# Kernel optimization log

Measured on AMD Instinct MI355X. Metric: run time of the kernel, lower is better.

The kernel has to match this reference:

```python
import jax, jax.numpy as jnp
import numpy as np

B, S, H, NH, I, V, P, T = 8, 512, 768, 12, 3072, 30522, 512, 2
D = H // NH
EPS = 1e-12


def _ln(x, g, b):
    m = x.mean(-1, keepdims=True)
    v = ((x - m) ** 2).mean(-1, keepdims=True)
    return (x - m) / jnp.sqrt(v + EPS) * g + b


def setup_inputs() -> dict:
    key = jax.random.key(0)
    ks = jax.random.split(key, 24)
    s = 0.02
    f32 = jnp.float32
    d = {
        'x': jax.random.randint(ks[0], (B, S), 0, V, dtype=jnp.int32),
        'W_word': (jax.random.normal(ks[1], (V, H)) * s).astype(f32),
        'W_pos': (jax.random.normal(ks[2], (P, H)) * s).astype(f32),
        'W_type': (jax.random.normal(ks[3], (T, H)) * s).astype(f32),
        'g_emb': jnp.ones((H,), f32), 'b_emb': jnp.zeros((H,), f32),
        'Wq': (jax.random.normal(ks[4], (H, H)) * s).astype(f32), 'bq': jnp.zeros((H,), f32),
        'Wk': (jax.random.normal(ks[5], (H, H)) * s).astype(f32), 'bk': jnp.zeros((H,), f32),
        'Wv': (jax.random.normal(ks[6], (H, H)) * s).astype(f32), 'bv': jnp.zeros((H,), f32),
        'Wo': (jax.random.normal(ks[7], (H, H)) * s).astype(f32), 'bo': jnp.zeros((H,), f32),
        'g_attn': jnp.ones((H,), f32), 'b_attn': jnp.zeros((H,), f32),
        'Wi': (jax.random.normal(ks[8], (H, I)) * s).astype(f32), 'bi': jnp.zeros((I,), f32),
        'Wd': (jax.random.normal(ks[9], (I, H)) * s).astype(f32), 'bd': jnp.zeros((H,), f32),
        'g_out': jnp.ones((H,), f32), 'b_out': jnp.zeros((H,), f32),
        'Wp': (jax.random.normal(ks[10], (H, H)) * s).astype(f32), 'bp': jnp.zeros((H,), f32),
    }
    return d


def _forward(x, W_word, W_pos, W_type, g_emb, b_emb, Wq, bq, Wk, bk, Wv, bv,
             Wo, bo, g_attn, b_attn, Wi, bi, Wd, bd, g_out, b_out, Wp, bp):
    # embeddings: word + position(arange) + token_type(all zeros -> row 0)
    h = W_word[x] + W_pos[jnp.arange(S)][None, :, :] + W_type[0][None, None, :]
    h = _ln(h, g_emb, b_emb)
    scale = 1.0 / jnp.sqrt(jnp.float32(D))
    # NOTE: the torch module shares one set of layer weights across all 6 layers.
    for _ in range(6):
        q = (h @ Wq + bq).reshape(B, S, NH, D).transpose(0, 2, 1, 3)  # bhsd
        k = (h @ Wk + bk).reshape(B, S, NH, D).transpose(0, 2, 1, 3)
        v = (h @ Wv + bv).reshape(B, S, NH, D).transpose(0, 2, 1, 3)
        scores = jnp.einsum('bhqd,bhkd->bhqk', q, k) * scale
        probs = jax.nn.softmax(scores, axis=-1)
        ctx = jnp.einsum('bhqk,bhkd->bhqd', probs, v)
        ctx = ctx.transpose(0, 2, 1, 3).reshape(B, S, H)
        attn = ctx @ Wo + bo
        xa = _ln(h + attn, g_attn, b_attn)
        ff = jax.nn.gelu(xa @ Wi + bi, approximate=False) @ Wd + bd
        h = _ln(xa + ff, g_out, b_out)
    pooled = h[:, 0, :] @ Wp + bp  # no tanh in the original module
    return h, pooled


def reference(x, W_word, W_pos, W_type, g_emb, b_emb, Wq, bq, Wk, bk, Wv, bv,
              Wo, bo, g_attn, b_attn, Wi, bi, Wd, bd, g_out, b_out, Wp, bp):
    return _forward(x, W_word, W_pos, W_type, g_emb, b_emb, Wq, bq, Wk, bk, Wv, bv,
                    Wo, bo, g_attn, b_attn, Wi, bi, Wd, bd, g_out, b_out, Wp, bp)
```

## Files before the change

kernel.cpp:

```cpp
#include <hip/hip_runtime.h>
#include <hip/hip_bf16.h>
#include <math.h>

#define B_  8
#define S_  512
#define H_  768
#define NH_ 12
#define D_  64
#define I_  3072
#define NTOK (B_*S_)
#define LDQ 2304

typedef __attribute__((ext_vector_type(8))) __bf16 bf16x8;
typedef __attribute__((ext_vector_type(8))) unsigned short ushort8;
typedef __attribute__((ext_vector_type(4))) float  f32x4;

__device__ __forceinline__ float gelu_exact(float x) {
    return 0.5f * x * (1.0f + erff(x * 0.70710678118654752440f));
}

__device__ __forceinline__ unsigned short f2bf(float x) {
    __hip_bfloat16 h = __float2bfloat16(x);
    return *reinterpret_cast<unsigned short*>(&h);
}

__device__ __forceinline__ void gload16(const void* g, void* l) {
    __builtin_amdgcn_global_load_lds(
        (const __attribute__((address_space(1))) void*)g,
        (__attribute__((address_space(3))) void*)l,
        16, 0, 0);
}

__global__ void cvtT_kernel(const float* __restrict__ W, __hip_bfloat16* __restrict__ WT,
                            int K, int N) {
    __shared__ float tile[32][33];
    int k0 = blockIdx.y * 32, n0 = blockIdx.x * 32;
    int tx = threadIdx.x & 31, ty = threadIdx.x >> 5;
    #pragma unroll
    for (int i = 0; i < 32; i += 8)
        tile[ty + i][tx] = W[(long)(k0 + ty + i) * N + n0 + tx];
    __syncthreads();
    #pragma unroll
    for (int i = 0; i < 32; i += 8)
        WT[(long)(n0 + ty + i) * K + k0 + tx] = __float2bfloat16(tile[tx][ty + i]);
}

__global__ void embed_ln_kernel(const int* __restrict__ ids,
                                const float* __restrict__ Wword,
                                const float* __restrict__ Wpos,
                                const float* __restrict__ Wtype,
                                const float* __restrict__ g,
                                const float* __restrict__ b,
                                float* __restrict__ out,
                                __hip_bfloat16* __restrict__ outb) {
    int t = blockIdx.x;
    int s = t % S_;
    long id = ids[t];
    int tid = threadIdx.x;
    float vals[3];
    float sum = 0.f, sq = 0.f;
    #pragma unroll
    for (int i = 0; i < 3; ++i) {
        int c = tid + 256 * i;
        float e = Wword[id * H_ + c] + Wpos[(long)s * H_ + c] + Wtype[c];
        vals[i] = e; sum += e; sq += e * e;
    }
    __shared__ float r1[256], r2[256];
    r1[tid] = sum; r2[tid] = sq; __syncthreads();
    for (int st = 128; st > 0; st >>= 1) {
        if (tid < st) { r1[tid] += r1[tid + st]; r2[tid] += r2[tid + st]; }
        __syncthreads();
    }
    float mean = r1[0] * (1.0f / H_);
    float var  = r2[0] * (1.0f / H_) - mean * mean;
    float inv  = rsqrtf(var + 1e-12f);
    #pragma unroll
    for (int i = 0; i < 3; ++i) {
        int c = tid + 256 * i;
        float v = (vals[i] - mean) * inv * g[c] + b[c];
        out[(long)t * H_ + c] = v;
        outb[(long)t * H_ + c] = __float2bfloat16(v);
    }
}

__global__ void add_ln_kernel(const float* __restrict__ a,
                              const float* __restrict__ r,
                              const float* __restrict__ g,
                              const float* __restrict__ bb,
                              float* __restrict__ out,
                              __hip_bfloat16* __restrict__ outb) {
    int t = blockIdx.x;
    int tid = threadIdx.x;
    float vals[3];
    float sum = 0.f, sq = 0.f;
    #pragma unroll
    for (int i = 0; i < 3; ++i) {
        int c = tid + 256 * i;
        float e = a[(long)t * H_ + c] + r[(long)t * H_ + c];
        vals[i] = e; sum += e; sq += e * e;
    }
    __shared__ float r1[256], r2[256];
    r1[tid] = sum; r2[tid] = sq; __syncthreads();
    for (int st = 128; st > 0; st >>= 1) {
        if (tid < st) { r1[tid] += r1[tid + st]; r2[tid] += r2[tid + st]; }
        __syncthreads();
    }
    float mean = r1[0] * (1.0f / H_);
    float var  = r2[0] * (1.0f / H_) - mean * mean;
    float inv  = rsqrtf(var + 1e-12f);
    #pragma unroll
    for (int i = 0; i < 3; ++i) {
        int c = tid + 256 * i;
        float v = (vals[i] - mean) * inv * g[c] + bb[c];
        out[(long)t * H_ + c] = v;
        outb[(long)t * H_ + c] = __float2bfloat16(v);
    }
}

template<int BM, int BN, int MI, int NJ, int ACT, int WF32, int WB16>
__global__ __launch_bounds__(256, 3) void mfma_gemm_kernel(
    const __hip_bfloat16* __restrict__ A,
    const __hip_bfloat16* __restrict__ BT,
    const float* __restrict__ bias,
    float* __restrict__ Cf,
    __hip_bfloat16* __restrict__ Cb,
    int M, int N, int K) {
    constexpr int WC = BN / (NJ * 16);
    constexpr int WR = BM / (MI * 16);
    static_assert(WR * WC == 4, "4 waves");
    constexpr int LA = BM * 4 / 256;
    constexpr int LB = BN * 4 / 256;
    constexpr int L  = LA + LB;
    __shared__ __align__(16) __hip_bfloat16 sA[2][BM * 32];
    __shared__ __align__(16) __hip_bfloat16 sB[2][BN * 32];
    const int tid  = threadIdx.x;
    const int lane = tid & 63;
    const int w    = tid >> 6;
    const int wr   = w / WC, wc = w % WC;
    const int l15  = lane & 15, l4 = lane >> 4;
    const int m0 = blockIdx.y * BM, n0 = blockIdx.x * BN;

    auto stage = [&](int buf, int k0) {
        #pragma unroll
        for (int t = 0; t < LA; ++t) {
            int c = tid + 256 * t;
            gload16(A + (long)(m0 + (c >> 2)) * K + k0 + (c & 3) * 8, &sA[buf][c * 8]);
        }
        #pragma unroll
        for (int t = 0; t < LB; ++t) {
            int c = tid + 256 * t;
            gload16(BT + (long)(n0 + (c >> 2)) * K + k0 + (c & 3) * 8, &sB[buf][c * 8]);
        }
    };

    f32x4 acc[MI][NJ] = {};
    const int nk = K >> 5;

    stage(0, 0);
    for (int t = 0; t < nk; ++t) {
        const int cur = t & 1;
        if (t + 1 < nk) {
            stage(cur ^ 1, (t + 1) * 32);
            asm volatile("s_waitcnt vmcnt(%0)" :: "i"(L) : "memory");
        } else {
            asm volatile("s_waitcnt vmcnt(0)" ::: "memory");
        }
        __builtin_amdgcn_sched_barrier(0);
        __builtin_amdgcn_s_barrier();
        __builtin_amdgcn_sched_barrier(0);

        const int kk = l4 * 8;
        bf16x8 af[MI], bf[NJ];
        #pragma unroll
        for (int i = 0; i < MI; ++i)
            af[i] = *reinterpret_cast<const bf16x8*>(&sA[cur][(wr * MI * 16 + i * 16 + l15) * 32 + kk]);
        #pragma unroll
        for (int j = 0; j < NJ; ++j)
            bf[j] = *reinterpret_cast<const bf16x8*>(&sB[cur][(wc * NJ * 16 + j * 16 + l15) * 32 + kk]);
        #pragma unroll
        for (int i = 0; i < MI; ++i)
            #pragma unroll
            for (int j = 0; j < NJ; ++j)
                acc[i][j] = __builtin_amdgcn_mfma_f32_16x16x32_bf16(af[i], bf[j], acc[i][j], 0, 0, 0);

        __builtin_amdgcn_sched_barrier(0);
        __builtin_amdgcn_s_barrier();
        __builtin_amdgcn_sched_barrier(0);
    }

    #pragma unroll
    for (int i = 0; i < MI; ++i) {
        #pragma unroll
        for (int j = 0; j < NJ; ++j) {
            int col = n0 + wc * NJ * 16 + j * 16 + l15;
            float bv = bias[col];
            #pragma unroll
            for (int r = 0; r < 4; ++r) {
                int row = m0 + wr * MI * 16 + i * 16 + l4 * 4 + r;
                float v = acc[i][j][r] + bv;
                if (ACT == 1) v = gelu_exact(v);
                if (WF32) Cf[(long)row * N + col] = v;
                if (WB16) Cb[(long)row * N + col] = __float2bfloat16(v);
            }
        }
    }
}

__global__ __launch_bounds__(256, 4) void flash_attn_kernel(
    const __hip_bfloat16* __restrict__ QKV,
    __hip_bfloat16* __restrict__ Ctx) {
    __shared__ __align__(16) unsigned short sK[64 * 72];
    __shared__ __align__(16) unsigned short sVt[64 * 72];
    __shared__ __align__(16) unsigned short sP[4 * 16 * 72];

    const int tid  = threadIdx.x;
    const int lane = tid & 63;
    const int w    = tid >> 6;
    const int l15  = lane & 15, l4 = lane >> 4;
    const int qb = blockIdx.x;
    const int bh = blockIdx.y;
    const int b  = bh / NH_, hd = bh % NH_;
    const long rbase = (long)b * S_ * LDQ;
    const int qoff = hd * D_, koff = H_ + hd * D_, voff = 2 * H_ + hd * D_;

    const int qrow0 = qb * 64 + w * 16;
    bf16x8 af[2];
    #pragma unroll
    for (int ks = 0; ks < 2; ++ks)
        af[ks] = *reinterpret_cast<const bf16x8*>(
            QKV + rbase + (long)(qrow0 + l15) * LDQ + qoff + ks * 32 + l4 * 8);

    f32x4 ctx[4] = {};
    float m_run[4], l_run[4];
    #pragma unroll
    for (int r = 0; r < 4; ++r) { m_run[r] = -1e30f; l_run[r] = 0.f; }

    const int sr = tid >> 2;
    const int sc = (tid & 3) * 16;
    unsigned short* pl = sP + w * (16 * 72);

    for (int kv0 = 0; kv0 < S_; kv0 += 64) {
        const __hip_bfloat16* kg = QKV + rbase + (long)(kv0 + sr) * LDQ + koff + sc;
        const __hip_bfloat16* vg = QKV + rbase + (long)(kv0 + sr) * LDQ + voff + sc;
        ushort8 kv_a = *reinterpret_cast<const ushort8*>(kg);
        ushort8 kv_b = *reinterpret_cast<const ushort8*>(kg + 8);
        ushort8 vv_a = *reinterpret_cast<const ushort8*>(vg);
        ushort8 vv_b = *reinterpret_cast<const ushort8*>(vg + 8);
        __syncthreads();
        *reinterpret_cast<ushort8*>(sK + sr * 72 + sc)     = kv_a;
        *reinterpret_cast<ushort8*>(sK + sr * 72 + sc + 8) = kv_b;
        #pragma unroll
        for (int i = 0; i < 8; ++i) {
            sVt[(sc + i) * 72 + sr]     = vv_a[i];
            sVt[(sc + 8 + i) * 72 + sr] = vv_b[i];
        }
        __syncthreads();

        f32x4 s[4];
        #pragma unroll
        for (int j = 0; j < 4; ++j) {
            s[j] = (f32x4){0.f, 0.f, 0.f, 0.f};
            #pragma unroll
            for (int ks = 0; ks < 2; ++ks) {
                bf16x8 bk = *reinterpret_cast<const bf16x8*>(sK + (j * 16 + l15) * 72 + ks * 32 + l4 * 8);
                s[j] = __builtin_amdgcn_mfma_f32_16x16x32_bf16(af[ks], bk, s[j], 0, 0, 0);
            }
        }
        #pragma unroll
        for (int j = 0; j < 4; ++j) s[j] *= 0.125f;

        #pragma unroll
        for (int r = 0; r < 4; ++r) {
            float mx = fmaxf(fmaxf(s[0][r], s[1][r]), fmaxf(s[2][r], s[3][r]));
            #pragma unroll
            for (int o = 1; o < 16; o <<= 1) mx = fmaxf(mx, __shfl_xor(mx, o));
            float mnew = fmaxf(m_run[r], mx);
            float sum = 0.f;
            #pragma unroll
            for (int j = 0; j < 4; ++j) {
                float p = __expf(s[j][r] - mnew);
                s[j][r] = p; sum += p;
            }
            #pragma unroll
            for (int o = 1; o < 16; o <<= 1) sum += __shfl_xor(sum, o);
            float resc = __expf(m_run[r] - mnew);
            l_run[r] = l_run[r] * resc + sum;
            m_run[r] = mnew;
            #pragma unroll
            for (int j = 0; j < 4; ++j) ctx[j][r] *= resc;
        }

        #pragma unroll
        for (int j = 0; j < 4; ++j)
            #pragma unroll
            for (int r = 0; r < 4; ++r)
                pl[(l4 * 4 + r) * 72 + j * 16 + l15] = f2bf(s[j][r]);

        #pragma unroll
        for (int ks = 0; ks < 2; ++ks) {
            bf16x8 ap = *reinterpret_cast<const bf16x8*>(pl + l15 * 72 + ks * 32 + l4 * 8);
            #pragma unroll
            for (int jd = 0; jd < 4; ++jd) {
                bf16x8 bv = *reinterpret_cast<const bf16x8*>(sVt + (jd * 16 + l15) * 72 + ks * 32 + l4 * 8);
                ctx[jd] = __builtin_amdgcn_mfma_f32_16x16x32_bf16(ap, bv, ctx[jd], 0, 0, 0);
            }
        }
    }

    #pragma unroll
    for (int r = 0; r < 4; ++r) {
        float inv = 1.f / l_run[r];
        long tok = (long)b * S_ + qb * 64 + w * 16 + l4 * 4 + r;
        #pragma unroll
        for (int jd = 0; jd < 4; ++jd)
            Ctx[tok * H_ + hd * D_ + jd * 16 + l15] = __float2bfloat16(ctx[jd][r] * inv);
    }
}

__global__ void pooled_kernel(const float* __restrict__ h,
                              const float* __restrict__ Wp,
                              const float* __restrict__ bp,
                              float* __restrict__ out) {
    int b = blockIdx.y;
    int col = blockIdx.x * 256 + threadIdx.x;
    const float* hb = h + (long)b * S_ * H_;
    float acc = 0.f;
    #pragma unroll 8
    for (int k = 0; k < H_; ++k)
        acc += hb[k] * Wp[(long)k * H_ + col];
    out[(long)b * H_ + col] = acc + bp[col];
}

extern "C" void kernel_launch(void* const* d_in, const int* in_sizes, int n_in,
                              void* d_out, int out_size, void* d_ws, size_t ws_size,
                              hipStream_t stream) {
    const int*   x      = (const int*)  d_in[0];
    const float* W_word = (const float*)d_in[1];
    const float* W_pos  = (const float*)d_in[2];
    const float* W_type = (const float*)d_in[3];
    const float* g_emb  = (const float*)d_in[4];
    const float* b_emb  = (const float*)d_in[5];
    const float* Wq     = (const float*)d_in[6];
    const float* bq     = (const float*)d_in[7];
    const float* Wk     = (const float*)d_in[8];
    const float* bk     = (const float*)d_in[9];
    const float* Wv     = (const float*)d_in[10];
    const float* bv     = (const float*)d_in[11];
    const float* Wo     = (const float*)d_in[12];
    const float* bo     = (const float*)d_in[13];
    const float* g_attn = (const float*)d_in[14];
    const float* b_attn = (const float*)d_in[15];
    const float* Wi     = (const float*)d_in[16];
    const float* bi     = (const float*)d_in[17];
    const float* Wd     = (const float*)d_in[18];
    const float* bd     = (const float*)d_in[19];
    const float* g_out  = (const float*)d_in[20];
    const float* b_out  = (const float*)d_in[21];
    const float* Wp     = (const float*)d_in[22];
    const float* bp     = (const float*)d_in[23];

    const size_t NT = (size_t)NTOK * H_;
    char* base = (char*)d_ws;
    size_t off = 0;
    auto alloc = [&](size_t bytes) -> char* {
        char* p = base + off;
        off += (bytes + 255) & ~(size_t)255;
        return p;
    };
    float* h    = (float*)alloc(NT * 4);
    float* xa   = (float*)alloc(NT * 4);
    float* kb   = (float*)alloc(NT * 4);
    __hip_bfloat16* h_b   = (__hip_bfloat16*)alloc(NT * 2);
    __hip_bfloat16* xa_b  = (__hip_bfloat16*)alloc(NT * 2);
    __hip_bfloat16* qkv_b = (__hip_bfloat16*)alloc((size_t)NTOK * LDQ * 2);
    __hip_bfloat16* ctx_b = (__hip_bfloat16*)alloc(NT * 2);
    __hip_bfloat16* ff1_b = (__hip_bfloat16*)alloc((size_t)NTOK * I_ * 2);
    __hip_bfloat16* WqkvT = (__hip_bfloat16*)alloc((size_t)LDQ * H_ * 2);
    __hip_bfloat16* WoT = (__hip_bfloat16*)alloc((size_t)H_ * H_ * 2);
    __hip_bfloat16* WiT = (__hip_bfloat16*)alloc((size_t)H_ * I_ * 2);
    __hip_bfloat16* WdT = (__hip_bfloat16*)alloc((size_t)I_ * H_ * 2);
    float* bqkv = (float*)alloc(LDQ * 4);

    cvtT_kernel<<<dim3(H_/32, H_/32), 256, 0, stream>>>(Wq, WqkvT, H_, H_);
    cvtT_kernel<<<dim3(H_/32, H_/32), 256, 0, stream>>>(Wk, WqkvT + (size_t)H_ * H_, H_, H_);
    cvtT_kernel<<<dim3(H_/32, H_/32), 256, 0, stream>>>(Wv, WqkvT + (size_t)2 * H_ * H_, H_, H_);
    cvtT_kernel<<<dim3(H_/32, H_/32), 256, 0, stream>>>(Wo, WoT, H_, H_);
    cvtT_kernel<<<dim3(I_/32, H_/32), 256, 0, stream>>>(Wi, WiT, H_, I_);
    cvtT_kernel<<<dim3(H_/32, I_/32), 256, 0, stream>>>(Wd, WdT, I_, H_);
    hipMemcpyAsync(bqkv,          bq, H_ * 4, hipMemcpyDeviceToDevice, stream);
    hipMemcpyAsync(bqkv + H_,     bk, H_ * 4, hipMemcpyDeviceToDevice, stream);
    hipMemcpyAsync(bqkv + 2 * H_, bv, H_ * 4, hipMemcpyDeviceToDevice, stream);

    embed_ln_kernel<<<NTOK, 256, 0, stream>>>(x, W_word, W_pos, W_type, g_emb, b_emb, h, h_b);

    dim3 gqkv(LDQ/128, NTOK/128);
    dim3 g768(H_/64,  NTOK/128);
    dim3 gi(I_/128,  NTOK/128);
    for (int layer = 0; layer < 6; ++layer) {
        mfma_gemm_kernel<128,128,4,4,0,0,1><<<gqkv, 256, 0, stream>>>(
            h_b, WqkvT, bqkv, nullptr, qkv_b, NTOK, LDQ, H_);
        flash_attn_kernel<<<dim3(S_/64, B_*NH_), 256, 0, stream>>>(qkv_b, ctx_b);
        mfma_gemm_kernel<128,64,4,2,0,1,0><<<g768, 256, 0, stream>>>(
            ctx_b, WoT, bo, kb, nullptr, NTOK, H_, H_);
        add_ln_kernel<<<NTOK, 256, 0, stream>>>(h, kb, g_attn, b_attn, xa, xa_b);
        mfma_gemm_kernel<128,128,4,4,1,0,1><<<gi, 256, 0, stream>>>(
            xa_b, WiT, bi, nullptr, ff1_b, NTOK, I_, H_);
        mfma_gemm_kernel<128,64,4,2,0,1,0><<<g768, 256, 0, stream>>>(
            ff1_b, WdT, bd, kb, nullptr, NTOK, H_, I_);
        add_ln_kernel<<<NTOK, 256, 0, stream>>>(xa, kb, g_out, b_out, h, h_b);
    }

    hipMemcpyAsync(d_out, h, NT * sizeof(float), hipMemcpyDeviceToDevice, stream);
    pooled_kernel<<<dim3(3, 8), 256, 0, stream>>>(h, Wp, bp, (float*)d_out + NT);
}
```

Before: 1.182 ms.

## Add 256x256 tiled MFMA GEMM with swizzled LDS for QKV and FFN1

Adds a 512-thread GEMM kernel that computes a 256x256 output tile per block. It double-buffers two 32-wide K sub-stages in 128KB of dynamic LDS, uses XOR-swizzled LDS addressing to reduce bank conflicts, and raises wave priority around the MFMA bursts. The QKV and FFN1 projections use it when the large LDS allocation is accepted; otherwise they fall back to the 128x128 kernel. The goal is more operand reuse per byte loaded. The cost is far fewer blocks (144 and 192), which may leave many of the 256 CUs idle at one block per CU.

Result: slower. 1.208 ms (+2.2%).

```diff
diff --git a/kernel.cpp b/kernel.cpp
--- a/kernel.cpp
+++ b/kernel.cpp
@@ -30,6 +30,8 @@
         (__attribute__((address_space(3))) void*)l,
         16, 0, 0);
 }
+
+#define SB0() __builtin_amdgcn_sched_barrier(0)
 
 __global__ void cvtT_kernel(const float* __restrict__ W, __hip_bfloat16* __restrict__ WT,
                             int K, int N) {
@@ -114,6 +116,109 @@
         float v = (vals[i] - mean) * inv * g[c] + bb[c];
         out[(long)t * H_ + c] = v;
         outb[(long)t * H_ + c] = __float2bfloat16(v);
+    }
+}
+
+template<int ACT, int WF32, int WB16>
+__global__ __launch_bounds__(512, 1) void mfma_gemm256_kernel(
+    const __hip_bfloat16* __restrict__ A,
+    const __hip_bfloat16* __restrict__ BT,
+    const float* __restrict__ bias,
+    float* __restrict__ Cf,
+    __hip_bfloat16* __restrict__ Cb,
+    int M, int N, int K) {
+    extern __shared__ __align__(16) unsigned short smem[];
+    const int tid  = threadIdx.x;
+    const int lane = tid & 63;
+    const int w    = tid >> 6;
+    const int wr   = w >> 2;
+    const int wc   = w & 3;
+    const int l15  = lane & 15, l4 = lane >> 4;
+    const int m0 = blockIdx.y * 256, n0 = blockIdx.x * 256;
+    const int goff = (l15 >> 1) & 3;
+
+    auto stageA = [&](int buf, int s, int k0) {
+        #pragma unroll
+        for (int u = 0; u < 2; ++u) {
+            int c = tid + 512 * u;
+            int row = c >> 2, gq = c & 3;
+            int gsrc = gq ^ ((row >> 1) & 3);
+            gload16(A + (long)(m0 + row) * K + k0 + s * 32 + gsrc * 8,
+                    smem + (buf * 2 + s) * 8192 + row * 32 + gq * 8);
+        }
+    };
+    auto stageB = [&](int buf, int s, int k0) {
+        #pragma unroll
+        for (int u = 0; u < 2; ++u) {
+            int c = tid + 512 * u;
+            int row = c >> 2, gq = c & 3;
+            int gsrc = gq ^ ((row >> 1) & 3);
+            gload16(BT + (long)(n0 + row) * K + k0 + s * 32 + gsrc * 8,
+                    smem + 32768 + (buf * 2 + s) * 8192 + row * 32 + gq * 8);
+        }
+    };
+
+    f32x4 acc[8][4] = {};
+
+    auto comp = [&](int buf, int s) {
+        const unsigned short* pa = smem + (buf * 2 + s) * 8192;
+        const unsigned short* pb = smem + 32768 + (buf * 2 + s) * 8192;
+        const int gsw = (l4 ^ goff) * 8;
+        bf16x8 afr[8], bfr[4];
+        #pragma unroll
+        for (int mi = 0; mi < 8; ++mi)
+            afr[mi] = *reinterpret_cast<const bf16x8*>(pa + (wr * 128 + mi * 16 + l15) * 32 + gsw);
+        #pragma unroll
+        for (int nj = 0; nj < 4; ++nj)
+            bfr[nj] = *reinterpret_cast<const bf16x8*>(pb + (wc * 64 + nj * 16 + l15) * 32 + gsw);
+        __builtin_amdgcn_s_setprio(1);
+        #pragma unroll
+        for (int mi = 0; mi < 8; ++mi)
+            #pragma unroll
+            for (int nj = 0; nj < 4; ++nj)
+                acc[mi][nj] = __builtin_amdgcn_mfma_f32_16x16x32_bf16(afr[mi], bfr[nj], acc[mi][nj], 0, 0, 0);
+        __builtin_amdgcn_s_setprio(0);
+    };
+
+    const int nt = K >> 6;
+    stageA(0, 0, 0); stageB(0, 0, 0);
+    stageA(0, 1, 0); stageB(0, 1, 0);
+    SB0(); asm volatile("s_waitcnt vmcnt(4)" ::: "memory");
+    SB0(); __builtin_amdgcn_s_barrier(); SB0();
+
+    for (int t = 0; t < nt; ++t) {
+        const int cur = t & 1;
+        const int kn = (t + 1) << 6;
+        const bool more = (t + 1 < nt);
+        if (more) { stageA(cur ^ 1, 0, kn); stageB(cur ^ 1, 0, kn); }
+        comp(cur, 0);
+        SB0();
+        if (more) asm volatile("s_waitcnt vmcnt(4)" ::: "memory");
+        else      asm volatile("s_waitcnt vmcnt(0)" ::: "memory");
+        SB0(); __builtin_amdgcn_s_barrier(); SB0();
+        if (more) { stageA(cur ^ 1, 1, kn); stageB(cur ^ 1, 1, kn); }
+        comp(cur, 1);
+        if (more) {
+            SB0(); asm volatile("s_waitcnt vmcnt(4)" ::: "memory");
+            SB0(); __builtin_amdgcn_s_barrier(); SB0();
+        }
+    }
+
+    #pragma unroll
+    for (int mi = 0; mi < 8; ++mi) {
+        #pragma unroll
+        for (int nj = 0; nj < 4; ++nj) {
+            int col = n0 + wc * 64 + nj * 16 + l15;
+            float bv = bias[col];
+            #pragma unroll
+            for (int r = 0; r < 4; ++r) {
+                int row = m0 + wr * 128 + mi * 16 + l4 * 4 + r;
+                float v = acc[mi][nj][r] + bv;
+                if (ACT == 1) v = gelu_exact(v);
+                if (WF32) Cf[(long)row * N + col] = v;
+                if (WB16) Cb[(long)row * N + col] = __float2bfloat16(v);
+            }
+        }
     }
 }
 
@@ -165,9 +270,7 @@
         } else {
             asm volatile("s_waitcnt vmcnt(0)" ::: "memory");
         }
-        __builtin_amdgcn_sched_barrier(0);
-        __builtin_amdgcn_s_barrier();
-        __builtin_amdgcn_sched_barrier(0);
+        SB0(); __builtin_amdgcn_s_barrier(); SB0();
 
         const int kk = l4 * 8;
         bf16x8 af[MI], bf[NJ];
@@ -183,9 +286,7 @@
             for (int j = 0; j < NJ; ++j)
                 acc[i][j] = __builtin_amdgcn_mfma_f32_16x16x32_bf16(af[i], bf[j], acc[i][j], 0, 0, 0);
 
-        __builtin_amdgcn_sched_barrier(0);
-        __builtin_amdgcn_s_barrier();
-        __builtin_amdgcn_sched_barrier(0);
+        SB0(); __builtin_amdgcn_s_barrier(); SB0();
     }
 
     #pragma unroll
@@ -393,18 +494,35 @@
 
     embed_ln_kernel<<<NTOK, 256, 0, stream>>>(x, W_word, W_pos, W_type, g_emb, b_emb, h, h_b);
 
-    dim3 gqkv(LDQ/128, NTOK/128);
-    dim3 g768(H_/64,  NTOK/128);
-    dim3 gi(I_/128,  NTOK/128);
+    const int SMEM = 131072;
+    hipError_t e1 = hipFuncSetAttribute((const void*)mfma_gemm256_kernel<0,0,1>,
+                                        hipFuncAttributeMaxDynamicSharedMemorySize, SMEM);
+    hipError_t e2 = hipFuncSetAttribute((const void*)mfma_gemm256_kernel<1,0,1>,
+                                        hipFuncAttributeMaxDynamicSharedMemorySize, SMEM);
+    const bool big = (e1 == hipSuccess) && (e2 == hipSuccess);
+
+    dim3 gqkv128(LDQ/128, NTOK/128);
+    dim3 gi128(I_/128, NTOK/128);
+    dim3 gqkv256(LDQ/256, NTOK/256);
+    dim3 gi256(I_/256, NTOK/256);
+    dim3 g768(H_/64, NTOK/128);
     for (int layer = 0; layer < 6; ++layer) {
-        mfma_gemm_kernel<128,128,4,4,0,0,1><<<gqkv, 256, 0, stream>>>(
-            h_b, WqkvT, bqkv, nullptr, qkv_b, NTOK, LDQ, H_);
+        if (big)
+            mfma_gemm256_kernel<0,0,1><<<gqkv256, 512, SMEM, stream>>>(
+                h_b, WqkvT, bqkv, nullptr, qkv_b, NTOK, LDQ, H_);
+        else
+            mfma_gemm_kernel<128,128,4,4,0,0,1><<<gqkv128, 256, 0, stream>>>(
+                h_b, WqkvT, bqkv, nullptr, qkv_b, NTOK, LDQ, H_);
         flash_attn_kernel<<<dim3(S_/64, B_*NH_), 256, 0, stream>>>(qkv_b, ctx_b);
         mfma_gemm_kernel<128,64,4,2,0,1,0><<<g768, 256, 0, stream>>>(
             ctx_b, WoT, bo, kb, nullptr, NTOK, H_, H_);
         add_ln_kernel<<<NTOK, 256, 0, stream>>>(h, kb, g_attn, b_attn, xa, xa_b);
-        mfma_gemm_kernel<128,128,4,4,1,0,1><<<gi, 256, 0, stream>>>(
-            xa_b, WiT, bi, nullptr, ff1_b, NTOK, I_, H_);
+        if (big)
+            mfma_gemm256_kernel<1,0,1><<<gi256, 512, SMEM, stream>>>(
+                xa_b, WiT, bi, nullptr, ff1_b, NTOK, I_, H_);
+        else
+            mfma_gemm_kernel<128,128,4,4,1,0,1><<<gi128, 256, 0, stream>>>(
+                xa_b, WiT, bi, nullptr, ff1_b, NTOK, I_, H_);
         mfma_gemm_kernel<128,64,4,2,0,1,0><<<g768, 256, 0, stream>>>(
             ff1_b, WdT, bd, kb, nullptr, NTOK, H_, I_);
         add_ln_kernel<<<NTOK, 256, 0, stream>>>(xa, kb, g_out, b_out, h, h_b);
```

## Triple-buffer GEMM LDS staging and XOR-swizzle LDS layout to avoid bank conflicts

Applied to the files above, without the earlier changes.

Moves the MFMA GEMM from double to triple buffering, so global-to-LDS loads for tile t+2 are issued while tile t is computed, with the vmcnt waits adjusted to match. It also XOR-swizzles the 16-byte chunk position within each 64-byte LDS row, so fragment reads by lanes with different rows hit different banks. The aim is to hide more memory latency and cut LDS bank conflicts. In exchange, LDS use per block grows by half, which may reduce the number of resident blocks (launch bounds ask for 3).

Measured after the change: 1.179 ms. No clear change (-0.3%).

```diff
diff --git a/kernel.cpp b/kernel.cpp
--- a/kernel.cpp
+++ b/kernel.cpp
@@ -30,6 +30,8 @@
         (__attribute__((address_space(3))) void*)l,
         16, 0, 0);
 }
+
+#define SB0() __builtin_amdgcn_sched_barrier(0)
 
 __global__ void cvtT_kernel(const float* __restrict__ W, __hip_bfloat16* __restrict__ WT,
                             int K, int N) {
@@ -131,25 +133,30 @@
     constexpr int LA = BM * 4 / 256;
     constexpr int LB = BN * 4 / 256;
     constexpr int L  = LA + LB;
-    __shared__ __align__(16) __hip_bfloat16 sA[2][BM * 32];
-    __shared__ __align__(16) __hip_bfloat16 sB[2][BN * 32];
+    __shared__ __align__(16) __hip_bfloat16 sA[3][BM * 32];
+    __shared__ __align__(16) __hip_bfloat16 sB[3][BN * 32];
     const int tid  = threadIdx.x;
     const int lane = tid & 63;
     const int w    = tid >> 6;
     const int wr   = w / WC, wc = w % WC;
     const int l15  = lane & 15, l4 = lane >> 4;
     const int m0 = blockIdx.y * BM, n0 = blockIdx.x * BN;
+    const int goff = (l15 >> 1) & 3;
 
     auto stage = [&](int buf, int k0) {
         #pragma unroll
         for (int t = 0; t < LA; ++t) {
             int c = tid + 256 * t;
-            gload16(A + (long)(m0 + (c >> 2)) * K + k0 + (c & 3) * 8, &sA[buf][c * 8]);
+            int row = c >> 2, gq = c & 3;
+            int gsrc = gq ^ ((row >> 1) & 3);
+            gload16(A + (long)(m0 + row) * K + k0 + gsrc * 8, &sA[buf][row * 32 + gq * 8]);
         }
         #pragma unroll
         for (int t = 0; t < LB; ++t) {
             int c = tid + 256 * t;
-            gload16(BT + (long)(n0 + (c >> 2)) * K + k0 + (c & 3) * 8, &sB[buf][c * 8]);
+            int row = c >> 2, gq = c & 3;
+            int gsrc = gq ^ ((row >> 1) & 3);
+            gload16(BT + (long)(n0 + row) * K + k0 + gsrc * 8, &sB[buf][row * 32 + gq * 8]);
         }
     };
 
@@ -157,35 +164,34 @@
     const int nk = K >> 5;
 
     stage(0, 0);
+    if (nk > 1) stage(1, 32);
     for (int t = 0; t < nk; ++t) {
-        const int cur = t & 1;
-        if (t + 1 < nk) {
-            stage(cur ^ 1, (t + 1) * 32);
+        const int cur = t % 3;
+        if (t + 2 < nk) {
+            stage((t + 2) % 3, (t + 2) * 32);
+            asm volatile("s_waitcnt vmcnt(%0)" :: "i"(2 * L) : "memory");
+        } else if (t + 1 < nk) {
             asm volatile("s_waitcnt vmcnt(%0)" :: "i"(L) : "memory");
         } else {
             asm volatile("s_waitcnt vmcnt(0)" ::: "memory");
         }
-        __builtin_amdgcn_sched_barrier(0);
-        __builtin_amdgcn_s_barrier();
-        __builtin_amdgcn_sched_barrier(0);
-
-        const int kk = l4 * 8;
+        SB0(); __builtin_amdgcn_s_barrier(); SB0();
+
+        const int gsw = (l4 ^ goff) * 8;
         bf16x8 af[MI], bf[NJ];
         #pragma unroll
         for (int i = 0; i < MI; ++i)
-            af[i] = *reinterpret_cast<const bf16x8*>(&sA[cur][(wr * MI * 16 + i * 16 + l15) * 32 + kk]);
+            af[i] = *reinterpret_cast<const bf16x8*>(&sA[cur][(wr * MI * 16 + i * 16 + l15) * 32 + gsw]);
         #pragma unroll
         for (int j = 0; j < NJ; ++j)
-            bf[j] = *reinterpret_cast<const bf16x8*>(&sB[cur][(wc * NJ * 16 + j * 16 + l15) * 32 + kk]);
+            bf[j] = *reinterpret_cast<const bf16x8*>(&sB[cur][(wc * NJ * 16 + j * 16 + l15) * 32 + gsw]);
         #pragma unroll
         for (int i = 0; i < MI; ++i)
             #pragma unroll
             for (int j = 0; j < NJ; ++j)
                 acc[i][j] = __builtin_amdgcn_mfma_f32_16x16x32_bf16(af[i], bf[j], acc[i][j], 0, 0, 0);
 
-        __builtin_amdgcn_sched_barrier(0);
-        __builtin_amdgcn_s_barrier();
-        __builtin_amdgcn_sched_barrier(0);
+        SB0(); __builtin_amdgcn_s_barrier(); SB0();
     }
 
     #pragma unroll
@@ -394,8 +400,8 @@
     embed_ln_kernel<<<NTOK, 256, 0, stream>>>(x, W_word, W_pos, W_type, g_emb, b_emb, h, h_b);
 
     dim3 gqkv(LDQ/128, NTOK/128);
-    dim3 g768(H_/64,  NTOK/128);
-    dim3 gi(I_/128,  NTOK/128);
+    dim3 gi(I_/128, NTOK/128);
+    dim3 g768(H_/64, NTOK/128);
     for (int layer = 0; layer < 6; ++layer) {
         mfma_gemm_kernel<128,128,4,4,0,0,1><<<gqkv, 256, 0, stream>>>(
             h_b, WqkvT, bqkv, nullptr, qkv_b, NTOK, LDQ, H_);
```
